# Kernel tuning notes

Hardware: AMD Instinct MI355X
Metric: run time of the kernel (lower is better)

## Reference

```python
import jax, jax.numpy as jnp
import numpy as np

NOISE_EPS = 0.01
TOP_K = 2


def setup_inputs() -> dict:
    key = jax.random.key(0)
    k1, k2, k3, k4 = jax.random.split(key, 4)
    B, S, D, E = 4, 4096, 2048, 64
    x = jax.random.normal(k1, (B, S, D), dtype=jnp.float32)
    raw_noise = jax.random.normal(k2, (B, S, E), dtype=jnp.float32)
    # gating_mlp: single Linear(D -> E), init std=0.02, zero bias
    W_gate = 0.02 * jax.random.normal(k3, (E, D), dtype=jnp.float32)
    b_gate = jnp.zeros((E,), dtype=jnp.float32)
    # noise_projection: Linear(D -> E, bias=False), init std=1/sqrt(D)
    W_noise = (1.0 / np.sqrt(D)) * jax.random.normal(k4, (E, D), dtype=jnp.float32)
    return {"x": x, "raw_noise": raw_noise, "W_gate": W_gate, "b_gate": b_gate, "W_noise": W_noise}


def reference(x, raw_noise, W_gate, b_gate, W_noise):
    # gate logits: [B,S,E]
    logits = jnp.einsum("bsd,ed->bse", x, W_gate) + b_gate
    # noisy top-k routing (training path)
    noise_stddev = jax.nn.softplus(jnp.einsum("bsd,ed->bse", x, W_noise)) + NOISE_EPS
    noisy = logits + raw_noise * noise_stddev
    top_v, top_i = jax.lax.top_k(noisy, TOP_K)            # [B,S,K]
    top_p = jax.nn.softmax(top_v.astype(jnp.float32), axis=-1).astype(noisy.dtype)
    B, S, E = noisy.shape
    T = B * S
    flat_logits = noisy.reshape(T, E)
    flat_i = top_i.reshape(T, TOP_K)
    flat_p = top_p.reshape(T, TOP_K)
    sparse = jnp.zeros((T, E), dtype=noisy.dtype).at[jnp.arange(T)[:, None], flat_i].set(flat_p)
    # aux load-balancing loss
    indicator = (sparse > 0.0).astype(jnp.float32)
    fraction_routed = indicator.sum(axis=0) / T           # f_e
    router_probs = jax.nn.softmax(flat_logits.astype(jnp.float32), axis=-1)
    avg_prob = router_probs.mean(axis=0)                  # p_e
    aux_loss = jnp.sum(fraction_routed * avg_prob) * E
    return sparse.reshape(B, S, E), aux_loss.astype(noisy.dtype)
```

## Files before the change

### kernel.cpp

```cpp
#include <hip/hip_runtime.h>
#include <math.h>

#define TOK 16384
#define DD  2048
#define EE  64
#define MT  32
#define BK  32
#define NKC 32

typedef _Float16 half8  __attribute__((ext_vector_type(8)));
typedef float    floatx4 __attribute__((ext_vector_type(4)));

__global__ void build_wf(const float* __restrict__ Wg, const float* __restrict__ Wn,
                         _Float16* __restrict__ wf) {
  int tid  = blockIdx.x * 256 + threadIdx.x;
  int lane = tid & 63;
  int kc   = (tid >> 6) & 63;
  int ct   = tid >> 12;
  int col  = (ct & 3) * 16 + (lane & 15);
  int k    = kc * 32 + (lane >> 4) * 8;
  const float* W = (ct < 4) ? Wg : Wn;
  const float* src = W + (size_t)col * DD + k;
  float4 a = *reinterpret_cast<const float4*>(src);
  float4 b = *reinterpret_cast<const float4*>(src + 4);
  float v[8] = {a.x, a.y, a.z, a.w, b.x, b.y, b.z, b.w};
  half8 hi, lo;
#pragma unroll
  for (int j = 0; j < 8; ++j) {
    _Float16 h = (_Float16)v[j];
    hi[j] = h;
    lo[j] = (_Float16)(v[j] - (float)h);
  }
  size_t base = (((size_t)(ct * 64 + kc) * 2 + 0) * 64 + lane) * 8;
  *reinterpret_cast<half8*>(wf + base)       = hi;
  *reinterpret_cast<half8*>(wf + base + 512) = lo;
}

__global__ __launch_bounds__(256, 2)
void gating_kernel(const float* __restrict__ x, const float* __restrict__ rn,
                   const _Float16* __restrict__ wf, const float* __restrict__ bg,
                   float* __restrict__ out,
                   float* __restrict__ cnt_g, float* __restrict__ psum_g) {
  __shared__ char smem[34432];
  float* Pacc = (float*)smem;
  float* Vb   = (float*)(smem + 16896);
  float* Eb   = (float*)(smem + 25344);
  float* isum = (float*)(smem + 33792);
  int*   ti   = (int*)(smem + 33920);
  float* tp   = (float*)(smem + 34176);

  const int t  = threadIdx.x;
  const int w  = t >> 6;
  const int ch = w & 1;
  const int kh = w >> 1;
  const int l  = t & 63;
  const int q  = l >> 4;
  const int cl = l & 15;
  const int t0 = blockIdx.x * MT;

  const float* xr0 = x + (size_t)(t0 + cl) * DD + kh * (NKC * BK) + q * 8;
  const float* xr1 = xr0 + (size_t)16 * DD;
  const half8* wfp = (const half8*)wf;
  const int cts[4] = {2 * ch, 2 * ch + 1, 4 + 2 * ch, 5 + 2 * ch};

  floatx4 acc[2][4];
#pragma unroll
  for (int mt = 0; mt < 2; ++mt)
#pragma unroll
    for (int j = 0; j < 4; ++j) acc[mt][j] = (floatx4)0.f;

  float4 xr[2][2][2];
  half8  Bf[2][4][2];

#define LOAD_CHUNK(kc, p)                                                        \
  {                                                                              \
    const int off = (kc) * BK;                                                   \
    xr[p][0][0] = *reinterpret_cast<const float4*>(xr0 + off);                   \
    xr[p][0][1] = *reinterpret_cast<const float4*>(xr0 + off + 4);               \
    xr[p][1][0] = *reinterpret_cast<const float4*>(xr1 + off);                   \
    xr[p][1][1] = *reinterpret_cast<const float4*>(xr1 + off + 4);               \
    const int kcg = kh * NKC + (kc);                                             \
    _Pragma("unroll")                                                            \
    for (int j = 0; j < 4; ++j) {                                                \
      _Pragma("unroll")                                                          \
      for (int s = 0; s < 2; ++s)                                                \
        Bf[p][j][s] = wfp[((size_t)(cts[j] * 64 + kcg) * 2 + s) * 64 + l];       \
    }                                                                            \
  }

  LOAD_CHUNK(0, 0)

#pragma unroll 2
  for (int kc = 0; kc < NKC; ++kc) {
    const int cur = kc & 1;
    if (kc + 1 < NKC) LOAD_CHUNK(kc + 1, cur ^ 1)

    half8 Ah[2], Al[2];
#pragma unroll
    for (int mt = 0; mt < 2; ++mt) {
      float v[8] = {xr[cur][mt][0].x, xr[cur][mt][0].y, xr[cur][mt][0].z, xr[cur][mt][0].w,
                    xr[cur][mt][1].x, xr[cur][mt][1].y, xr[cur][mt][1].z, xr[cur][mt][1].w};
#pragma unroll
      for (int j = 0; j < 8; ++j) {
        _Float16 h = (_Float16)v[j];
        Ah[mt][j] = h;
        Al[mt][j] = (_Float16)(v[j] - (float)h);
      }
    }
#pragma unroll
    for (int mt = 0; mt < 2; ++mt)
#pragma unroll
      for (int j = 0; j < 4; ++j)
        acc[mt][j] = __builtin_amdgcn_mfma_f32_16x16x32_f16(Ah[mt], Bf[cur][j][0], acc[mt][j], 0, 0, 0);
#pragma unroll
    for (int mt = 0; mt < 2; ++mt)
#pragma unroll
      for (int j = 0; j < 4; ++j)
        acc[mt][j] = __builtin_amdgcn_mfma_f32_16x16x32_f16(Ah[mt], Bf[cur][j][1], acc[mt][j], 0, 0, 0);
#pragma unroll
    for (int mt = 0; mt < 2; ++mt)
#pragma unroll
      for (int j = 0; j < 4; ++j)
        acc[mt][j] = __builtin_amdgcn_mfma_f32_16x16x32_f16(Al[mt], Bf[cur][j][0], acc[mt][j], 0, 0, 0);
  }
#undef LOAD_CHUNK

  if (kh == 1) {
#pragma unroll
    for (int mt = 0; mt < 2; ++mt)
#pragma unroll
      for (int j = 0; j < 4; ++j) {
        const int cf = ((j >> 1) ? 64 : 0) + ch * 32 + (j & 1) * 16 + cl;
#pragma unroll
        for (int r = 0; r < 4; ++r)
          Pacc[(mt * 16 + q * 4 + r) * 132 + cf] = acc[mt][j][r];
      }
  }
  __syncthreads();

  if (kh == 0) {
    float bgv[2], rnv[2][4][2];
#pragma unroll
    for (int j = 0; j < 2; ++j) bgv[j] = bg[ch * 32 + j * 16 + cl];
#pragma unroll
    for (int mt = 0; mt < 2; ++mt)
#pragma unroll
      for (int r = 0; r < 4; ++r)
#pragma unroll
        for (int j = 0; j < 2; ++j)
          rnv[mt][r][j] = rn[(size_t)(t0 + mt * 16 + q * 4 + r) * EE + ch * 32 + j * 16 + cl];

#pragma unroll
    for (int mt = 0; mt < 2; ++mt)
#pragma unroll
      for (int r = 0; r < 4; ++r) {
        const int tk = mt * 16 + q * 4 + r;
#pragma unroll
        for (int j = 0; j < 2; ++j) {
          const int cg = ch * 32 + j * 16 + cl;
          float g  = acc[mt][j][r]     + Pacc[tk * 132 + cg]      + bgv[j];
          float h  = acc[mt][j + 2][r] + Pacc[tk * 132 + 64 + cg];
          float sp = (h > 20.f) ? h : log1pf(expf(h));
          float v  = g + rnv[mt][r][j] * (sp + 0.01f);
          Vb[tk * 66 + cg] = v;
          Eb[tk * 66 + cg] = expf(v);
        }
      }
  }
  __syncthreads();

  if (t < MT) {
    float v1 = -1e30f, v2 = -1e30f;
    int   i1 = 0, i2 = 0;
    float s = 0.f;
    for (int e = 0; e < EE; ++e) {
      float v = Vb[t * 66 + e];
      s += Eb[t * 66 + e];
      if (v > v1)      { v2 = v1; i2 = i1; v1 = v; i1 = e; }
      else if (v > v2) { v2 = v;  i2 = e; }
    }
    isum[t] = 1.f / s;
    ti[t * 2 + 0] = i1; ti[t * 2 + 1] = i2;
    float e2 = expf(v2 - v1);
    float dn = 1.f + e2;
    tp[t * 2 + 0] = 1.f / dn;
    tp[t * 2 + 1] = e2 / dn;
  }
  __syncthreads();

  {
    const int m  = t >> 3;
    const int c0 = (t & 7) * 8;
    const int i1 = ti[m * 2 + 0], i2 = ti[m * 2 + 1];
    const float p1 = tp[m * 2 + 0], p2 = tp[m * 2 + 1];
    float o[8];
#pragma unroll
    for (int j = 0; j < 8; ++j) {
      const int col = c0 + j;
      o[j] = (col == i1) ? p1 : ((col == i2) ? p2 : 0.f);
    }
    float* dst = out + (size_t)(t0 + m) * EE + c0;
    *reinterpret_cast<float4*>(dst)     = make_float4(o[0], o[1], o[2], o[3]);
    *reinterpret_cast<float4*>(dst + 4) = make_float4(o[4], o[5], o[6], o[7]);
  }

  if (t < EE) {
    float s = 0.f;
    int   cn = 0;
#pragma unroll
    for (int m = 0; m < MT; ++m) {
      s  += Eb[m * 66 + t] * isum[m];
      cn += (ti[m * 2 + 0] == t) + (ti[m * 2 + 1] == t);
    }
    atomicAdd(&psum_g[t], s);
    atomicAdd(&cnt_g[t], (float)cn);
  }
}

__global__ void aux_kernel(const float* __restrict__ cnt_g,
                           const float* __restrict__ psum_g,
                           float* __restrict__ out) {
  int e = threadIdx.x;
  float v = cnt_g[e] * psum_g[e];
#pragma unroll
  for (int o = 32; o > 0; o >>= 1) v += __shfl_down(v, o);
  if (e == 0)
    out[(size_t)TOK * EE] = v * ((float)EE / ((float)TOK * (float)TOK));
}

extern "C" void kernel_launch(void* const* d_in, const int* in_sizes, int n_in,
                              void* d_out, int out_size, void* d_ws, size_t ws_size,
                              hipStream_t stream) {
  const float* x  = (const float*)d_in[0];
  const float* rn = (const float*)d_in[1];
  const float* Wg = (const float*)d_in[2];
  const float* bg = (const float*)d_in[3];
  const float* Wn = (const float*)d_in[4];
  float* out    = (float*)d_out;
  float* cnt_g  = (float*)d_ws;
  float* psum_g = cnt_g + EE;
  _Float16* wf  = (_Float16*)((float*)d_ws + 128);

  hipMemsetAsync(d_ws, 0, 2 * EE * sizeof(float), stream);
  build_wf<<<128, 256, 0, stream>>>(Wg, Wn, wf);
  gating_kernel<<<TOK / MT, 256, 0, stream>>>(x, rn, wf, bg, out, cnt_g, psum_g);
  aux_kernel<<<1, 64, 0, stream>>>(cnt_g, psum_g, out);
}
```

Before: 250.2 us.

## Stage x and weight fragments through LDS with async loads, 64-token tiles

The gating GEMM now stages x rows and the precomputed fp16 hi/lo weight fragments into double-buffered shared memory with global_load_lds. The x tile uses an XOR-swizzled layout to avoid bank conflicts. The tile grows to 64 tokens with 512 threads, and the split-K across waves plus its shared-memory partial-sum reduction is removed, so each wave owns 16 gate and 16 noise columns for 32 tokens. The aim is to halve how often the weights are re-read per token and to replace per-thread register loads with cooperative async copies. The cost is a block barrier every K chunk and larger shared-memory use, which may reduce occupancy.

```diff
diff --git a/kernel.cpp b/kernel.cpp
--- a/kernel.cpp
+++ b/kernel.cpp
@@ -4,12 +4,16 @@
 #define TOK 16384
 #define DD  2048
 #define EE  64
-#define MT  32
+#define MT  64
 #define BK  32
-#define NKC 32
+#define NKC 64
 
 typedef _Float16 half8  __attribute__((ext_vector_type(8)));
 typedef float    floatx4 __attribute__((ext_vector_type(4)));
+
+#define GLD16(g, l) __builtin_amdgcn_global_load_lds(                          \
+    (__attribute__((address_space(1))) const void*)(g),                        \
+    (__attribute__((address_space(3))) void*)(l), 16, 0, 0)
 
 __global__ void build_wf(const float* __restrict__ Wg, const float* __restrict__ Wn,
                          _Float16* __restrict__ wf) {
@@ -36,137 +40,109 @@
   *reinterpret_cast<half8*>(wf + base + 512) = lo;
 }
 
-__global__ __launch_bounds__(256, 2)
+__global__ __launch_bounds__(512, 2)
 void gating_kernel(const float* __restrict__ x, const float* __restrict__ rn,
                    const _Float16* __restrict__ wf, const float* __restrict__ bg,
                    float* __restrict__ out,
                    float* __restrict__ cnt_g, float* __restrict__ psum_g) {
-  __shared__ char smem[34432];
-  float* Pacc = (float*)smem;
-  float* Vb   = (float*)(smem + 16896);
-  float* Eb   = (float*)(smem + 25344);
+  __shared__ char smem[49152];
+  float* Vb   = (float*)smem;
+  float* Eb   = (float*)(smem + 16896);
   float* isum = (float*)(smem + 33792);
-  int*   ti   = (int*)(smem + 33920);
-  float* tp   = (float*)(smem + 34176);
+  int*   ti   = (int*)(smem + 34048);
+  float* tp   = (float*)(smem + 34560);
 
   const int t  = threadIdx.x;
   const int w  = t >> 6;
-  const int ch = w & 1;
-  const int kh = w >> 1;
   const int l  = t & 63;
   const int q  = l >> 4;
   const int cl = l & 15;
+  const int cg = w & 3;
+  const int mh = w >> 2;
+  const int c  = cg * 16 + cl;
   const int t0 = blockIdx.x * MT;
 
-  const float* xr0 = x + (size_t)(t0 + cl) * DD + kh * (NKC * BK) + q * 8;
-  const float* xr1 = xr0 + (size_t)16 * DD;
-  const half8* wfp = (const half8*)wf;
-  const int cts[4] = {2 * ch, 2 * ch + 1, 4 + 2 * ch, 5 + 2 * ch};
-
-  floatx4 acc[2][4];
-#pragma unroll
-  for (int mt = 0; mt < 2; ++mt)
-#pragma unroll
-    for (int j = 0; j < 4; ++j) acc[mt][j] = (floatx4)0.f;
-
-  float4 xr[2][2][2];
-  half8  Bf[2][4][2];
-
-#define LOAD_CHUNK(kc, p)                                                        \
-  {                                                                              \
-    const int off = (kc) * BK;                                                   \
-    xr[p][0][0] = *reinterpret_cast<const float4*>(xr0 + off);                   \
-    xr[p][0][1] = *reinterpret_cast<const float4*>(xr0 + off + 4);               \
-    xr[p][1][0] = *reinterpret_cast<const float4*>(xr1 + off);                   \
-    xr[p][1][1] = *reinterpret_cast<const float4*>(xr1 + off + 4);               \
-    const int kcg = kh * NKC + (kc);                                             \
-    _Pragma("unroll")                                                            \
-    for (int j = 0; j < 4; ++j) {                                                \
-      _Pragma("unroll")                                                          \
-      for (int s = 0; s < 2; ++s)                                                \
-        Bf[p][j][s] = wfp[((size_t)(cts[j] * 64 + kcg) * 2 + s) * 64 + l];       \
-    }                                                                            \
-  }
-
-  LOAD_CHUNK(0, 0)
-
-#pragma unroll 2
+  const int su = l >> 3;
+  const int sv = l & 7;
+  const float* xg = x + (size_t)(t0 + w * 8 + su) * DD + ((sv ^ su) * 4);
+  const _Float16* bsrc0 = wf + (size_t)l * 8;
+
+#define STAGE(kc_, p_)                                                         \
+  {                                                                            \
+    char* bX = smem + (p_) * 24576;                                            \
+    GLD16(xg + (kc_) * BK, bX + w * 1024);                                     \
+    const _Float16* bs = bsrc0 + ((size_t)(w * 64 + (kc_)) * 2) * 512;         \
+    GLD16(bs,       bX + 8192 + (2 * w) * 1024);                               \
+    GLD16(bs + 512, bX + 8192 + (2 * w + 1) * 1024);                           \
+  }
+
+  const float bgv = bg[c];
+  float rnv[2][4];
+#pragma unroll
+  for (int i = 0; i < 2; ++i)
+#pragma unroll
+    for (int r = 0; r < 4; ++r)
+      rnv[i][r] = rn[(size_t)(t0 + (mh * 2 + i) * 16 + q * 4 + r) * EE + c];
+
+  floatx4 accg[2], accn[2];
+#pragma unroll
+  for (int i = 0; i < 2; ++i) { accg[i] = (floatx4)0.f; accn[i] = (floatx4)0.f; }
+
+  STAGE(0, 0)
+
   for (int kc = 0; kc < NKC; ++kc) {
-    const int cur = kc & 1;
-    if (kc + 1 < NKC) LOAD_CHUNK(kc + 1, cur ^ 1)
-
-    half8 Ah[2], Al[2];
-#pragma unroll
-    for (int mt = 0; mt < 2; ++mt) {
-      float v[8] = {xr[cur][mt][0].x, xr[cur][mt][0].y, xr[cur][mt][0].z, xr[cur][mt][0].w,
-                    xr[cur][mt][1].x, xr[cur][mt][1].y, xr[cur][mt][1].z, xr[cur][mt][1].w};
+    const int p = kc & 1;
+    char* bufX = smem + p * 24576;
+    char* bufB = bufX + 8192;
+    __syncthreads();
+    if (kc + 1 < NKC) STAGE(kc + 1, p ^ 1)
+
+    half8 Bg[2], Bn[2];
+#pragma unroll
+    for (int s = 0; s < 2; ++s) {
+      Bg[s] = *reinterpret_cast<const half8*>(bufB + (cg * 2 + s) * 1024 + l * 16);
+      Bn[s] = *reinterpret_cast<const half8*>(bufB + ((4 + cg) * 2 + s) * 1024 + l * 16);
+    }
+#pragma unroll
+    for (int i = 0; i < 2; ++i) {
+      const int row = (mh * 2 + i) * 16 + cl;
+      const int r7  = row & 7;
+      const float4 g0 = *reinterpret_cast<const float4*>(
+          bufX + row * 128 + (((2 * q) ^ r7) << 4));
+      const float4 g1 = *reinterpret_cast<const float4*>(
+          bufX + row * 128 + (((2 * q + 1) ^ r7) << 4));
+      float vv[8] = {g0.x, g0.y, g0.z, g0.w, g1.x, g1.y, g1.z, g1.w};
+      half8 Ah, Al;
 #pragma unroll
       for (int j = 0; j < 8; ++j) {
-        _Float16 h = (_Float16)v[j];
-        Ah[mt][j] = h;
-        Al[mt][j] = (_Float16)(v[j] - (float)h);
+        _Float16 h = (_Float16)vv[j];
+        Ah[j] = h;
+        Al[j] = (_Float16)(vv[j] - (float)h);
       }
-    }
-#pragma unroll
-    for (int mt = 0; mt < 2; ++mt)
-#pragma unroll
-      for (int j = 0; j < 4; ++j)
-        acc[mt][j] = __builtin_amdgcn_mfma_f32_16x16x32_f16(Ah[mt], Bf[cur][j][0], acc[mt][j], 0, 0, 0);
-#pragma unroll
-    for (int mt = 0; mt < 2; ++mt)
-#pragma unroll
-      for (int j = 0; j < 4; ++j)
-        acc[mt][j] = __builtin_amdgcn_mfma_f32_16x16x32_f16(Ah[mt], Bf[cur][j][1], acc[mt][j], 0, 0, 0);
-#pragma unroll
-    for (int mt = 0; mt < 2; ++mt)
-#pragma unroll
-      for (int j = 0; j < 4; ++j)
-        acc[mt][j] = __builtin_amdgcn_mfma_f32_16x16x32_f16(Al[mt], Bf[cur][j][0], acc[mt][j], 0, 0, 0);
-  }
-#undef LOAD_CHUNK
-
-  if (kh == 1) {
-#pragma unroll
-    for (int mt = 0; mt < 2; ++mt)
-#pragma unroll
-      for (int j = 0; j < 4; ++j) {
-        const int cf = ((j >> 1) ? 64 : 0) + ch * 32 + (j & 1) * 16 + cl;
-#pragma unroll
-        for (int r = 0; r < 4; ++r)
-          Pacc[(mt * 16 + q * 4 + r) * 132 + cf] = acc[mt][j][r];
-      }
-  }
+      accg[i] = __builtin_amdgcn_mfma_f32_16x16x32_f16(Ah, Bg[0], accg[i], 0, 0, 0);
+      accn[i] = __builtin_amdgcn_mfma_f32_16x16x32_f16(Ah, Bn[0], accn[i], 0, 0, 0);
+      accg[i] = __builtin_amdgcn_mfma_f32_16x16x32_f16(Ah, Bg[1], accg[i], 0, 0, 0);
+      accn[i] = __builtin_amdgcn_mfma_f32_16x16x32_f16(Ah, Bn[1], accn[i], 0, 0, 0);
+      accg[i] = __builtin_amdgcn_mfma_f32_16x16x32_f16(Al, Bg[0], accg[i], 0, 0, 0);
+      accn[i] = __builtin_amdgcn_mfma_f32_16x16x32_f16(Al, Bn[0], accn[i], 0, 0, 0);
+    }
+  }
+#undef STAGE
+
   __syncthreads();
 
-  if (kh == 0) {
-    float bgv[2], rnv[2][4][2];
-#pragma unroll
-    for (int j = 0; j < 2; ++j) bgv[j] = bg[ch * 32 + j * 16 + cl];
-#pragma unroll
-    for (int mt = 0; mt < 2; ++mt)
-#pragma unroll
-      for (int r = 0; r < 4; ++r)
-#pragma unroll
-        for (int j = 0; j < 2; ++j)
-          rnv[mt][r][j] = rn[(size_t)(t0 + mt * 16 + q * 4 + r) * EE + ch * 32 + j * 16 + cl];
-
-#pragma unroll
-    for (int mt = 0; mt < 2; ++mt)
-#pragma unroll
-      for (int r = 0; r < 4; ++r) {
-        const int tk = mt * 16 + q * 4 + r;
-#pragma unroll
-        for (int j = 0; j < 2; ++j) {
-          const int cg = ch * 32 + j * 16 + cl;
-          float g  = acc[mt][j][r]     + Pacc[tk * 132 + cg]      + bgv[j];
-          float h  = acc[mt][j + 2][r] + Pacc[tk * 132 + 64 + cg];
-          float sp = (h > 20.f) ? h : log1pf(expf(h));
-          float v  = g + rnv[mt][r][j] * (sp + 0.01f);
-          Vb[tk * 66 + cg] = v;
-          Eb[tk * 66 + cg] = expf(v);
-        }
-      }
-  }
+#pragma unroll
+  for (int i = 0; i < 2; ++i)
+#pragma unroll
+    for (int r = 0; r < 4; ++r) {
+      const int tk = (mh * 2 + i) * 16 + q * 4 + r;
+      float g  = accg[i][r] + bgv;
+      float h  = accn[i][r];
+      float sp = (h > 20.f) ? h : log1pf(expf(h));
+      float v  = g + rnv[i][r] * (sp + 0.01f);
+      Vb[tk * 66 + c] = v;
+      Eb[tk * 66 + c] = expf(v);
+    }
   __syncthreads();
 
   if (t < MT) {
@@ -243,6 +219,6 @@
 
   hipMemsetAsync(d_ws, 0, 2 * EE * sizeof(float), stream);
   build_wf<<<128, 256, 0, stream>>>(Wg, Wn, wf);
-  gating_kernel<<<TOK / MT, 256, 0, stream>>>(x, rn, wf, bg, out, cnt_g, psum_g);
+  gating_kernel<<<TOK / MT, 512, 0, stream>>>(x, rn, wf, bg, out, cnt_g, psum_g);
   aux_kernel<<<1, 64, 0, stream>>>(cnt_g, psum_g, out);
 }
```

Measured after the change: 257.4 us. 1.03x slower.

## Stage split-fp16 x tiles through LDS with 16-token blocks and higher occupancy

Applied to the files above, without the earlier changes.

The gating kernel now handles 16 tokens per block instead of 32 and targets 4 blocks per SM instead of 2. Each thread converts its slice of x to hi/lo fp16 once and writes it into a double-buffered LDS tile, so each element is split once rather than per wave. The router-noise and bias loads are hoisted ahead of the main loop. In exchange, each K step needs a __syncthreads, and the W fragments are reloaded for half as many tokens, which doubles total weight traffic from L2.

```diff
diff --git a/kernel.cpp b/kernel.cpp
--- a/kernel.cpp
+++ b/kernel.cpp
@@ -4,10 +4,12 @@
 #define TOK 16384
 #define DD  2048
 #define EE  64
-#define MT  32
+#define MT  16
 #define BK  32
 #define NKC 32
-
+#define LDA 40
+
+typedef _Float16 half4v __attribute__((ext_vector_type(4)));
 typedef _Float16 half8  __attribute__((ext_vector_type(8)));
 typedef float    floatx4 __attribute__((ext_vector_type(4)));
 
@@ -36,18 +38,19 @@
   *reinterpret_cast<half8*>(wf + base + 512) = lo;
 }
 
-__global__ __launch_bounds__(256, 2)
+__global__ __launch_bounds__(256, 4)
 void gating_kernel(const float* __restrict__ x, const float* __restrict__ rn,
                    const _Float16* __restrict__ wf, const float* __restrict__ bg,
                    float* __restrict__ out,
                    float* __restrict__ cnt_g, float* __restrict__ psum_g) {
-  __shared__ char smem[34432];
-  float* Pacc = (float*)smem;
-  float* Vb   = (float*)(smem + 16896);
-  float* Eb   = (float*)(smem + 25344);
-  float* isum = (float*)(smem + 33792);
-  int*   ti   = (int*)(smem + 33920);
-  float* tp   = (float*)(smem + 34176);
+  __shared__ char smem[19008];
+  _Float16* xs  = (_Float16*)smem;
+  float*    Pacc= (float*)smem;
+  float*    Vb  = (float*)(smem + 10240);
+  float*    Eb  = (float*)(smem + 14464);
+  float*    isum= (float*)(smem + 18688);
+  int*      ti  = (int*)(smem + 18752);
+  float*    tp  = (float*)(smem + 18880);
 
   const int t  = threadIdx.x;
   const int w  = t >> 6;
@@ -58,114 +61,119 @@
   const int cl = l & 15;
   const int t0 = blockIdx.x * MT;
 
-  const float* xr0 = x + (size_t)(t0 + cl) * DD + kh * (NKC * BK) + q * 8;
-  const float* xr1 = xr0 + (size_t)16 * DD;
+  const int skh  = t >> 7;
+  const int stok = (t >> 3) & 15;
+  const int skf  = (t & 7) * 4;
+  const float* xg = x + (size_t)(t0 + stok) * DD + skh * 1024 + skf;
+  const int sbase = skh * 1280 + stok * LDA + skf;
+
   const half8* wfp = (const half8*)wf;
   const int cts[4] = {2 * ch, 2 * ch + 1, 4 + 2 * ch, 5 + 2 * ch};
 
-  floatx4 acc[2][4];
-#pragma unroll
-  for (int mt = 0; mt < 2; ++mt)
-#pragma unroll
-    for (int j = 0; j < 4; ++j) acc[mt][j] = (floatx4)0.f;
-
-  float4 xr[2][2][2];
-  half8  Bf[2][4][2];
-
-#define LOAD_CHUNK(kc, p)                                                        \
-  {                                                                              \
-    const int off = (kc) * BK;                                                   \
-    xr[p][0][0] = *reinterpret_cast<const float4*>(xr0 + off);                   \
-    xr[p][0][1] = *reinterpret_cast<const float4*>(xr0 + off + 4);               \
-    xr[p][1][0] = *reinterpret_cast<const float4*>(xr1 + off);                   \
-    xr[p][1][1] = *reinterpret_cast<const float4*>(xr1 + off + 4);               \
-    const int kcg = kh * NKC + (kc);                                             \
-    _Pragma("unroll")                                                            \
-    for (int j = 0; j < 4; ++j) {                                                \
-      _Pragma("unroll")                                                          \
-      for (int s = 0; s < 2; ++s)                                                \
-        Bf[p][j][s] = wfp[((size_t)(cts[j] * 64 + kcg) * 2 + s) * 64 + l];       \
-    }                                                                            \
-  }
-
-  LOAD_CHUNK(0, 0)
-
-#pragma unroll 2
+  float bgv[2] = {0.f, 0.f};
+  float rnv[4][2];
+#pragma unroll
+  for (int r = 0; r < 4; ++r) { rnv[r][0] = 0.f; rnv[r][1] = 0.f; }
+  if (kh == 0) {
+#pragma unroll
+    for (int j = 0; j < 2; ++j) bgv[j] = bg[ch * 32 + j * 16 + cl];
+#pragma unroll
+    for (int r = 0; r < 4; ++r)
+#pragma unroll
+      for (int j = 0; j < 2; ++j)
+        rnv[r][j] = rn[(size_t)(t0 + q * 4 + r) * EE + ch * 32 + j * 16 + cl];
+  }
+
+  floatx4 acc[4];
+#pragma unroll
+  for (int j = 0; j < 4; ++j) acc[j] = (floatx4)0.f;
+
+  {
+    float4 a = *reinterpret_cast<const float4*>(xg);
+    float v[4] = {a.x, a.y, a.z, a.w};
+    half4v hi, lo;
+#pragma unroll
+    for (int j = 0; j < 4; ++j) {
+      _Float16 h = (_Float16)v[j];
+      hi[j] = h;
+      lo[j] = (_Float16)(v[j] - (float)h);
+    }
+    *reinterpret_cast<half4v*>(&xs[sbase])       = hi;
+    *reinterpret_cast<half4v*>(&xs[sbase + 640]) = lo;
+  }
+
   for (int kc = 0; kc < NKC; ++kc) {
     const int cur = kc & 1;
-    if (kc + 1 < NKC) LOAD_CHUNK(kc + 1, cur ^ 1)
-
-    half8 Ah[2], Al[2];
-#pragma unroll
-    for (int mt = 0; mt < 2; ++mt) {
-      float v[8] = {xr[cur][mt][0].x, xr[cur][mt][0].y, xr[cur][mt][0].z, xr[cur][mt][0].w,
-                    xr[cur][mt][1].x, xr[cur][mt][1].y, xr[cur][mt][1].z, xr[cur][mt][1].w};
-#pragma unroll
-      for (int j = 0; j < 8; ++j) {
+    const bool more = (kc < NKC - 1);
+    float4 pa;
+    if (more) pa = *reinterpret_cast<const float4*>(xg + (kc + 1) * BK);
+    half8 B[4][2];
+    {
+      const int kcg = kh * NKC + kc;
+#pragma unroll
+      for (int j = 0; j < 4; ++j)
+#pragma unroll
+        for (int s = 0; s < 2; ++s)
+          B[j][s] = wfp[((size_t)(cts[j] * 64 + kcg) * 2 + s) * 64 + l];
+    }
+    __syncthreads();
+
+    const int abase = cur * 2560 + kh * 1280 + cl * LDA + q * 8;
+    half8 Ah = *reinterpret_cast<const half8*>(&xs[abase]);
+    half8 Al = *reinterpret_cast<const half8*>(&xs[abase + 640]);
+#pragma unroll
+    for (int j = 0; j < 4; ++j)
+      acc[j] = __builtin_amdgcn_mfma_f32_16x16x32_f16(Ah, B[j][0], acc[j], 0, 0, 0);
+#pragma unroll
+    for (int j = 0; j < 4; ++j)
+      acc[j] = __builtin_amdgcn_mfma_f32_16x16x32_f16(Ah, B[j][1], acc[j], 0, 0, 0);
+#pragma unroll
+    for (int j = 0; j < 4; ++j)
+      acc[j] = __builtin_amdgcn_mfma_f32_16x16x32_f16(Al, B[j][0], acc[j], 0, 0, 0);
+
+    if (more) {
+      float v[4] = {pa.x, pa.y, pa.z, pa.w};
+      half4v hi, lo;
+#pragma unroll
+      for (int j = 0; j < 4; ++j) {
         _Float16 h = (_Float16)v[j];
-        Ah[mt][j] = h;
-        Al[mt][j] = (_Float16)(v[j] - (float)h);
+        hi[j] = h;
+        lo[j] = (_Float16)(v[j] - (float)h);
       }
-    }
-#pragma unroll
-    for (int mt = 0; mt < 2; ++mt)
-#pragma unroll
-      for (int j = 0; j < 4; ++j)
-        acc[mt][j] = __builtin_amdgcn_mfma_f32_16x16x32_f16(Ah[mt], Bf[cur][j][0], acc[mt][j], 0, 0, 0);
-#pragma unroll
-    for (int mt = 0; mt < 2; ++mt)
-#pragma unroll
-      for (int j = 0; j < 4; ++j)
-        acc[mt][j] = __builtin_amdgcn_mfma_f32_16x16x32_f16(Ah[mt], Bf[cur][j][1], acc[mt][j], 0, 0, 0);
-#pragma unroll
-    for (int mt = 0; mt < 2; ++mt)
-#pragma unroll
-      for (int j = 0; j < 4; ++j)
-        acc[mt][j] = __builtin_amdgcn_mfma_f32_16x16x32_f16(Al[mt], Bf[cur][j][0], acc[mt][j], 0, 0, 0);
-  }
-#undef LOAD_CHUNK
+      const int nb = (cur ^ 1) * 2560 + sbase;
+      *reinterpret_cast<half4v*>(&xs[nb])       = hi;
+      *reinterpret_cast<half4v*>(&xs[nb + 640]) = lo;
+    }
+  }
+
+  __syncthreads();
 
   if (kh == 1) {
 #pragma unroll
-    for (int mt = 0; mt < 2; ++mt)
-#pragma unroll
-      for (int j = 0; j < 4; ++j) {
-        const int cf = ((j >> 1) ? 64 : 0) + ch * 32 + (j & 1) * 16 + cl;
-#pragma unroll
-        for (int r = 0; r < 4; ++r)
-          Pacc[(mt * 16 + q * 4 + r) * 132 + cf] = acc[mt][j][r];
+    for (int j = 0; j < 4; ++j) {
+      const int cf = ((j >> 1) ? 64 : 0) + ch * 32 + (j & 1) * 16 + cl;
+#pragma unroll
+      for (int r = 0; r < 4; ++r)
+        Pacc[(q * 4 + r) * 132 + cf] = acc[j][r];
+    }
+  }
+  __syncthreads();
+
+  if (kh == 0) {
+#pragma unroll
+    for (int r = 0; r < 4; ++r) {
+      const int tk = q * 4 + r;
+#pragma unroll
+      for (int j = 0; j < 2; ++j) {
+        const int cg = ch * 32 + j * 16 + cl;
+        float g  = acc[j][r]     + Pacc[tk * 132 + cg]      + bgv[j];
+        float h  = acc[j + 2][r] + Pacc[tk * 132 + 64 + cg];
+        float sp = (h > 20.f) ? h : log1pf(expf(h));
+        float v  = g + rnv[r][j] * (sp + 0.01f);
+        Vb[tk * 66 + cg] = v;
+        Eb[tk * 66 + cg] = expf(v);
       }
-  }
-  __syncthreads();
-
-  if (kh == 0) {
-    float bgv[2], rnv[2][4][2];
-#pragma unroll
-    for (int j = 0; j < 2; ++j) bgv[j] = bg[ch * 32 + j * 16 + cl];
-#pragma unroll
-    for (int mt = 0; mt < 2; ++mt)
-#pragma unroll
-      for (int r = 0; r < 4; ++r)
-#pragma unroll
-        for (int j = 0; j < 2; ++j)
-          rnv[mt][r][j] = rn[(size_t)(t0 + mt * 16 + q * 4 + r) * EE + ch * 32 + j * 16 + cl];
-
-#pragma unroll
-    for (int mt = 0; mt < 2; ++mt)
-#pragma unroll
-      for (int r = 0; r < 4; ++r) {
-        const int tk = mt * 16 + q * 4 + r;
-#pragma unroll
-        for (int j = 0; j < 2; ++j) {
-          const int cg = ch * 32 + j * 16 + cl;
-          float g  = acc[mt][j][r]     + Pacc[tk * 132 + cg]      + bgv[j];
-          float h  = acc[mt][j + 2][r] + Pacc[tk * 132 + 64 + cg];
-          float sp = (h > 20.f) ? h : log1pf(expf(h));
-          float v  = g + rnv[mt][r][j] * (sp + 0.01f);
-          Vb[tk * 66 + cg] = v;
-          Eb[tk * 66 + cg] = expf(v);
-        }
-      }
+    }
   }
   __syncthreads();
 
@@ -189,19 +197,18 @@
   __syncthreads();
 
   {
-    const int m  = t >> 3;
-    const int c0 = (t & 7) * 8;
+    const int m  = t >> 4;
+    const int c0 = (t & 15) * 4;
     const int i1 = ti[m * 2 + 0], i2 = ti[m * 2 + 1];
     const float p1 = tp[m * 2 + 0], p2 = tp[m * 2 + 1];
-    float o[8];
-#pragma unroll
-    for (int j = 0; j < 8; ++j) {
+    float o[4];
+#pragma unroll
+    for (int j = 0; j < 4; ++j) {
       const int col = c0 + j;
       o[j] = (col == i1) ? p1 : ((col == i2) ? p2 : 0.f);
     }
-    float* dst = out + (size_t)(t0 + m) * EE + c0;
-    *reinterpret_cast<float4*>(dst)     = make_float4(o[0], o[1], o[2], o[3]);
-    *reinterpret_cast<float4*>(dst + 4) = make_float4(o[4], o[5], o[6], o[7]);
+    *reinterpret_cast<float4*>(out + (size_t)(t0 + m) * EE + c0) =
+        make_float4(o[0], o[1], o[2], o[3]);
   }
 
   if (t < EE) {
```

Result: slower. 267.6 us (+6.9%).
